# Kernel tuning notes

Hardware: AMD Instinct MI355X
Metric: run time of the kernel (lower is better)

The kernel has to match this reference:

```python
import jax, jax.numpy as jnp
import numpy as np


def setup_inputs() -> dict:
    key = jax.random.key(0)
    ks = jax.random.split(key, 5)
    b, l, ns, ni, d = 128, 64, 32, 16, 256
    scale = 1.0 / np.sqrt(d)
    return {
        "token_features": jax.random.normal(ks[0], (b, l, d), jnp.float32),
        "w_route_ws": jax.random.normal(ks[1], (l, ns, d), jnp.float32) * scale,
        "w_pose_ws": jax.random.normal(ks[2], (l, ns, d, d), jnp.float32) * scale,
        "w_route_si": jax.random.normal(ks[3], (ns, ni, d), jnp.float32) * scale,
        "w_pose_si": jax.random.normal(ks[4], (ns, ni, d, d), jnp.float32) * scale,
    }


def reference(token_features, w_route_ws, w_pose_ws, w_route_si, w_pose_si):
    d_model = token_features.shape[-1]

    # ---- route words -> slots ----
    # token activations ('norm' strategy): mean over d_model -> (b, l)
    a_words = jnp.sum(token_features, axis=-1) / d_model
    # routing logits (b, l, n_slot_caps), softmax over slot caps
    c_ws = jax.nn.softmax(jnp.einsum('lnj,blj->bln', w_route_ws, token_features), axis=-1)
    weighted_c = jnp.einsum('bls,bl->bs', c_ws, a_words)            # (b, ns)
    a_slots = weighted_c / jnp.sum(a_words, axis=-1, keepdims=True)  # (b, ns)
    # pose votes (b, l, ns, d) then weighted aggregation + divisive normalization
    u_hat_slots = jnp.einsum('lnij,blj->blni', w_pose_ws, token_features)
    u_slots = jnp.einsum('bls,bl,blsk->bsk', c_ws, a_words, u_hat_slots) / weighted_c[:, :, None]

    # ---- route slots -> intents ----
    c_si = jax.nn.softmax(jnp.einsum('sij,bsj->bsi', w_route_si, u_slots), axis=-1)
    weighted_c2 = jnp.einsum('bsi,bs->bi', c_si, a_slots)            # (b, ni)
    a_intents = weighted_c2 / jnp.sum(a_slots, axis=-1, keepdims=True)
    u_hat_intents = jnp.einsum('sijk,bsk->bsik', w_pose_si, u_slots)  # (b, ns, ni, d)
    u_intents = jnp.einsum('bsi,bs,bsik->bik', c_si, a_slots, u_hat_intents) / weighted_c2[:, :, None]

    return a_slots, u_slots, a_intents, u_intents
```

## Files before the change

kernel.cpp:

```cpp
#include <hip/hip_runtime.h>
#include <math.h>

#define B  128
#define L  64
#define NS 32
#define NI 16
#define D  256

typedef __attribute__((ext_vector_type(8))) short bf16x8;
typedef __attribute__((ext_vector_type(4))) float f32x4;

__device__ __forceinline__ float wave_reduce_sum(float v) {
#pragma unroll
  for (int off = 32; off; off >>= 1) v += __shfl_xor(v, off, 64);
  return v;
}
__device__ __forceinline__ float wave_reduce_max(float v) {
#pragma unroll
  for (int off = 32; off; off >>= 1) v = fmaxf(v, __shfl_xor(v, off, 64));
  return v;
}

__device__ __forceinline__ uint cvt_pk_bf16(float a, float b) {
  uint r;
  asm("v_cvt_pk_bf16_f32 %0, %1, %2" : "=v"(r) : "v"(a), "v"(b));
  return r;
}
__device__ __forceinline__ void split4(float4 v, uint2& h, uint2& lo) {
  h.x = cvt_pk_bf16(v.x, v.y);
  h.y = cvt_pk_bf16(v.z, v.w);
  float h0 = __uint_as_float(h.x << 16);
  float h1 = __uint_as_float(h.x & 0xFFFF0000u);
  float h2 = __uint_as_float(h.y << 16);
  float h3 = __uint_as_float(h.y & 0xFFFF0000u);
  lo.x = cvt_pk_bf16(v.x - h0, v.y - h1);
  lo.y = cvt_pk_bf16(v.z - h2, v.w - h3);
}

#define LGKM_BARRIER()                                   \
  do {                                                   \
    asm volatile("s_waitcnt lgkmcnt(0)" ::: "memory");   \
    __builtin_amdgcn_s_barrier();                        \
    asm volatile("" ::: "memory");                       \
  } while (0)

__device__ __forceinline__ int swzA(int row, int kcol) {
  int byte = (row << 7) + (kcol << 1);
  byte ^= (row & 7) << 4;
  return byte >> 1;
}

__global__ __launch_bounds__(256) void k1_route_words(
    const float* __restrict__ tf, const float* __restrict__ wr,
    float* __restrict__ wlsT, float* __restrict__ a_words) {
  int bl = blockIdx.x;
  int b  = bl >> 6;
  int l  = bl & (L - 1);
  int t  = threadIdx.x;
  int wave = t >> 6, lane = t & 63;
  __shared__ float sx[D];
  __shared__ float slog[NS];
  __shared__ float s_aw;
  sx[t] = tf[bl * D + t];
  __syncthreads();
  const float* wbase = wr + l * NS * D;
#pragma unroll
  for (int r = 0; r < 8; ++r) {
    int n = wave * 8 + r;
    const float* w = wbase + n * D;
    float p = 0.f;
#pragma unroll
    for (int jj = 0; jj < 4; ++jj) {
      int j = lane + jj * 64;
      p = fmaf(w[j], sx[j], p);
    }
    p = wave_reduce_sum(p);
    if (lane == 0) slog[n] = p;
  }
  if (wave == 0) {
    float p = sx[lane] + sx[lane + 64] + sx[lane + 128] + sx[lane + 192];
    p = wave_reduce_sum(p);
    if (lane == 0) s_aw = p * (1.f / D);
  }
  __syncthreads();
  if (wave == 0) {
    float aw = s_aw;
    float v = (lane < NS) ? slog[lane] : -INFINITY;
    float m = wave_reduce_max(v);
    float e = (lane < NS) ? __expf(v - m) : 0.f;
    float s = wave_reduce_sum(e);
    if (lane < NS) wlsT[(l * NS + lane) * B + b] = (e / s) * aw;
    if (lane == 0) a_words[bl] = aw;
  }
}

__global__ __launch_bounds__(64) void k2_slots_agg(
    const float* __restrict__ wlsT, const float* __restrict__ a_words,
    float* __restrict__ weighted_c, float* __restrict__ a_slots) {
  int b = blockIdx.x;
  int lane = threadIdx.x;
  float aw = a_words[b * L + lane];
  float sa = wave_reduce_sum(aw);
  if (lane < NS) {
    float wc = 0.f;
    for (int l = 0; l < L; ++l) wc += wlsT[(l * NS + lane) * B + b];
    weighted_c[b * NS + lane] = wc;
    a_slots[b * NS + lane] = wc / sa;
  }
}

__global__ __launch_bounds__(256, 4) void k3_mfma(
    const float* __restrict__ tf, const float* __restrict__ wp,
    const float* __restrict__ wlsT, float* __restrict__ part, int nsplit) {
  __shared__ ushort Ah[128 * 64], Al[128 * 64];

  int bx  = blockIdx.x;
  int t   = threadIdx.x;
  int sp  = bx % nsplit;
  int rem = bx / nsplit;
  int it  = rem & 3;
  int s   = rem >> 2;
  int i0  = it * 64;
  int lchunk = L / nsplit;
  int l0     = sp * lchunk;
  int steps  = lchunk * 4;

  int lane = t & 63, wn = t >> 6;
  int fr = lane & 15, q = lane >> 4;
  int rw = t >> 4, jq = (t & 15) * 4;

  f32x4 acc[8];
#pragma unroll
  for (int mi = 0; mi < 8; ++mi) acc[mi] = (f32x4)0.f;

  const size_t wlo = (size_t)(i0 + wn * 16 + fr) * D + q * 8;

  float4 rW[4];
  auto loadW = [&](int step) {
    if (step >= steps) step = steps - 1;
    int l  = l0 + (step >> 2);
    int jc = (step & 3) * 64;
    const float* wb = wp + ((size_t)l * NS + s) * (D * D) + wlo + jc;
    rW[0] = *(const float4*)(wb);
    rW[1] = *(const float4*)(wb + 4);
    rW[2] = *(const float4*)(wb + 32);
    rW[3] = *(const float4*)(wb + 36);
  };
  loadW(0);

  for (int step = 0; step < steps; ++step) {
    int l  = l0 + (step >> 2);
    int jc = (step & 3) * 64;
    const float* ab = tf + (size_t)l * D + jc + jq;
    const float* sb = wlsT + ((size_t)l * NS + s) * B;
#pragma unroll
    for (int p = 0; p < 8; ++p) {
      int bb = p * 16 + rw;
      float4 v = *(const float4*)(ab + (size_t)bb * (L * D));
      float sc = sb[bb];
      v.x *= sc; v.y *= sc; v.z *= sc; v.w *= sc;
      uint2 h, lo;
      split4(v, h, lo);
      *(uint2*)&Ah[swzA(bb, jq)] = h;
      *(uint2*)&Al[swzA(bb, jq)] = lo;
    }
    bf16x8 bh[2], bl[2];
#pragma unroll
    for (int k2 = 0; k2 < 2; ++k2) {
      uint2 h0, l0u, h1, l1u;
      split4(rW[k2 * 2], h0, l0u);
      split4(rW[k2 * 2 + 1], h1, l1u);
      uint4 hu = {h0.x, h0.y, h1.x, h1.y};
      uint4 lu = {l0u.x, l0u.y, l1u.x, l1u.y};
      bh[k2] = __builtin_bit_cast(bf16x8, hu);
      bl[k2] = __builtin_bit_cast(bf16x8, lu);
    }
    loadW(step + 1);
    LGKM_BARRIER();
#pragma unroll
    for (int k2 = 0; k2 < 2; ++k2) {
      int kb = k2 * 32 + q * 8;
#pragma unroll
      for (int mi = 0; mi < 8; ++mi) {
        bf16x8 ah = *(const bf16x8*)&Ah[swzA(mi * 16 + fr, kb)];
        bf16x8 al = *(const bf16x8*)&Al[swzA(mi * 16 + fr, kb)];
        acc[mi] = __builtin_amdgcn_mfma_f32_16x16x32_bf16(ah, bh[k2], acc[mi], 0, 0, 0);
        acc[mi] = __builtin_amdgcn_mfma_f32_16x16x32_bf16(ah, bl[k2], acc[mi], 0, 0, 0);
        acc[mi] = __builtin_amdgcn_mfma_f32_16x16x32_bf16(al, bh[k2], acc[mi], 0, 0, 0);
      }
    }
    LGKM_BARRIER();
  }

  float* pout = part + ((size_t)sp * NS + s) * (B * D);
  int col = i0 + wn * 16 + fr;
#pragma unroll
  for (int mi = 0; mi < 8; ++mi)
#pragma unroll
    for (int r = 0; r < 4; ++r) {
      int bb = mi * 16 + q * 4 + r;
      pout[(size_t)bb * D + col] = acc[mi][r];
    }
}

__global__ __launch_bounds__(256) void k3r_reduce(
    const float* __restrict__ part, const float* __restrict__ wc,
    float* __restrict__ u_slots, int nsplit) {
  int idx = blockIdx.x * 256 + threadIdx.x;
  int i  = idx & (D - 1);
  int sb = idx >> 8;
  int b  = sb & (B - 1);
  int s  = sb >> 7;
  float v = 0.f;
  for (int sp = 0; sp < nsplit; ++sp)
    v += part[(size_t)sp * (NS * B * D) + idx];
  u_slots[((size_t)b * NS + s) * D + i] = v / wc[b * NS + s];
}

__global__ __launch_bounds__(64) void k4_route_si(
    const float* __restrict__ u_slots, const float* __restrict__ wr_si,
    const float* __restrict__ a_slots, float* __restrict__ w2) {
  int bs = blockIdx.x;
  int s  = bs & (NS - 1);
  int lane = threadIdx.x;
  __shared__ float su[D];
  __shared__ float slog[NI];
#pragma unroll
  for (int jj = 0; jj < 4; ++jj) su[lane + jj * 64] = u_slots[bs * D + lane + jj * 64];
  __syncthreads();
  for (int i = 0; i < NI; ++i) {
    const float* w = wr_si + (s * NI + i) * D;
    float p = 0.f;
#pragma unroll
    for (int jj = 0; jj < 4; ++jj) {
      int j = lane + jj * 64;
      p = fmaf(w[j], su[j], p);
    }
    p = wave_reduce_sum(p);
    if (lane == 0) slog[i] = p;
  }
  __syncthreads();
  float v = (lane < NI) ? slog[lane] : -INFINITY;
  float m = wave_reduce_max(v);
  float e = (lane < NI) ? __expf(v - m) : 0.f;
  float ssum = wave_reduce_sum(e);
  if (lane < NI) w2[bs * NI + lane] = (e / ssum) * a_slots[bs];
}

__global__ __launch_bounds__(64) void k5_intents_agg(
    const float* __restrict__ w2, const float* __restrict__ a_slots,
    float* __restrict__ wc2, float* __restrict__ a_intents) {
  int b = blockIdx.x;
  int lane = threadIdx.x;
  float as = (lane < NS) ? a_slots[b * NS + lane] : 0.f;
  float sas = wave_reduce_sum(as);
  if (lane < NI) {
    float wc = 0.f;
    for (int s = 0; s < NS; ++s) wc += w2[(b * NS + s) * NI + lane];
    wc2[b * NI + lane] = wc;
    a_intents[b * NI + lane] = wc / sas;
  }
}

__global__ __launch_bounds__(256) void k6_wsum(
    const float* __restrict__ wps, float* __restrict__ wsum) {
  __shared__ float red[4][D];
  int si = blockIdx.x;
  int t  = threadIdx.x;
  int k4 = (t & 63) * 4;
  int jg = t >> 6;
  const float* base = wps + (size_t)si * D * D;
  float4 acc = {0.f, 0.f, 0.f, 0.f};
  for (int j = jg; j < D; j += 4) {
    float4 v = *(const float4*)(base + (size_t)j * D + k4);
    acc.x += v.x; acc.y += v.y; acc.z += v.z; acc.w += v.w;
  }
  *(float4*)&red[jg][k4] = acc;
  __syncthreads();
  wsum[si * D + t] = (red[0][t] + red[1][t]) + (red[2][t] + red[3][t]);
}

__global__ __launch_bounds__(256) void k7_uintents(
    const float* __restrict__ u_slots, const float* __restrict__ w2,
    const float* __restrict__ wsum, const float* __restrict__ wc2,
    float* __restrict__ u_intents) {
  int bi = blockIdx.x;
  int b = bi >> 4, i = bi & (NI - 1);
  int k = threadIdx.x;
  float acc = 0.f;
  for (int s = 0; s < NS; ++s) {
    float w = w2[(b * NS + s) * NI + i];
    acc = fmaf(w * u_slots[(b * NS + s) * D + k], wsum[(s * NI + i) * D + k], acc);
  }
  u_intents[bi * D + k] = acc / wc2[bi];
}

extern "C" void kernel_launch(void* const* d_in, const int* in_sizes, int n_in,
                              void* d_out, int out_size, void* d_ws, size_t ws_size,
                              hipStream_t stream) {
  const float* tf    = (const float*)d_in[0];
  const float* wr_ws = (const float*)d_in[1];
  const float* wp_ws = (const float*)d_in[2];
  const float* wr_si = (const float*)d_in[3];
  const float* wp_si = (const float*)d_in[4];

  float* out       = (float*)d_out;
  float* a_slots   = out;
  float* u_slots   = a_slots + B * NS;
  float* a_intents = u_slots + B * NS * D;
  float* u_intents = a_intents + B * NI;

  float* ws         = (float*)d_ws;
  float* wlsT       = ws;
  float* a_words    = wlsT + L * NS * B;
  float* weighted_c = a_words + B * L;
  float* w2         = weighted_c + B * NS;
  float* wc2        = w2 + B * NS * NI;
  float* wsum       = wc2 + B * NI;
  float* part       = wsum + NS * NI * D;

  const size_t base_f  = 473088;
  const size_t chunk_f = (size_t)NS * B * D;
  size_t avail_f = ws_size / sizeof(float);
  int nsplit = 1;
  if (avail_f >= base_f + 8 * chunk_f)      nsplit = 8;
  else if (avail_f >= base_f + 4 * chunk_f) nsplit = 4;
  else if (avail_f >= base_f + 2 * chunk_f) nsplit = 2;

  k1_route_words<<<B * L, 256, 0, stream>>>(tf, wr_ws, wlsT, a_words);
  k2_slots_agg<<<B, 64, 0, stream>>>(wlsT, a_words, weighted_c, a_slots);
  k3_mfma<<<128 * nsplit, 256, 0, stream>>>(tf, wp_ws, wlsT, part, nsplit);
  k3r_reduce<<<(NS * B * D) / 256, 256, 0, stream>>>(part, weighted_c, u_slots, nsplit);
  k6_wsum<<<NS * NI, 256, 0, stream>>>(wp_si, wsum);
  k4_route_si<<<B * NS, 64, 0, stream>>>(u_slots, wr_si, a_slots, w2);
  k5_intents_agg<<<B, 64, 0, stream>>>(w2, a_slots, wc2, a_intents);
  k7_uintents<<<B * NI, 256, 0, stream>>>(u_slots, w2, wsum, wc2, u_intents);
}
```

Before: 277.6 us.

## Merge wsum reduction into MFMA kernel and double-buffer A tiles with 2x2 warp tiling

The pose-vote MFMA kernel now also carries the independent w_pose_si column-sum blocks, interleaved in one grid, so that memory-bound reduction can overlap with the compute-bound GEMM and one launch disappears. The GEMM is restructured with double-buffered LDS A tiles and register-prefetched A and W for two steps ahead. A 2x2 wave tiling (64 rows x 32 cols per wave) replaces the 128x16 per-wave layout to improve reuse. The L split drops from 8 to 4 and occupancy from 4 to 2 blocks per CU, which trades parallelism and latency hiding for more register buffering.

```diff
diff --git a/kernel.cpp b/kernel.cpp
--- a/kernel.cpp
+++ b/kernel.cpp
@@ -109,15 +109,51 @@
   }
 }
 
-__global__ __launch_bounds__(256, 4) void k3_mfma(
+#define ATILE 8192
+
+__global__ __launch_bounds__(256, 2) void k3k6(
     const float* __restrict__ tf, const float* __restrict__ wp,
-    const float* __restrict__ wlsT, float* __restrict__ part, int nsplit) {
-  __shared__ ushort Ah[128 * 64], Al[128 * 64];
-
-  int bx  = blockIdx.x;
-  int t   = threadIdx.x;
-  int sp  = bx % nsplit;
-  int rem = bx / nsplit;
+    const float* __restrict__ wlsT, const float* __restrict__ wps,
+    float* __restrict__ part, float* __restrict__ wsum,
+    int nsplit, int nk3) {
+  union Smem {
+    struct { ushort Ah[2 * ATILE], Al[2 * ATILE]; } k3;
+    struct { float red[4][D]; } k6;
+  };
+  __shared__ Smem sm;
+
+  int bx = blockIdx.x;
+  int t  = threadIdx.x;
+
+  bool isK6;
+  int idx;
+  if (nk3 == 512) {
+    isK6 = (bx & 1);
+    idx  = bx >> 1;
+  } else {
+    isK6 = bx < NS * NI;
+    idx  = isK6 ? bx : bx - NS * NI;
+  }
+
+  if (isK6) {
+    int si = idx;
+    int k4 = (t & 63) * 4;
+    int jg = t >> 6;
+    const float* base = wps + (size_t)si * D * D;
+    float4 acc = {0.f, 0.f, 0.f, 0.f};
+    for (int j = jg; j < D; j += 4) {
+      float4 v = *(const float4*)(base + (size_t)j * D + k4);
+      acc.x += v.x; acc.y += v.y; acc.z += v.z; acc.w += v.w;
+    }
+    *(float4*)&sm.k6.red[jg][k4] = acc;
+    __syncthreads();
+    wsum[si * D + t] = (sm.k6.red[0][t] + sm.k6.red[1][t]) +
+                       (sm.k6.red[2][t] + sm.k6.red[3][t]);
+    return;
+  }
+
+  int sp  = idx % nsplit;
+  int rem = idx / nsplit;
   int it  = rem & 3;
   int s   = rem >> 2;
   int i0  = it * 64;
@@ -125,81 +161,122 @@
   int l0     = sp * lchunk;
   int steps  = lchunk * 4;
 
-  int lane = t & 63, wn = t >> 6;
+  int lane = t & 63, wv = t >> 6;
+  int wm = wv >> 1, wn = wv & 1;
   int fr = lane & 15, q = lane >> 4;
   int rw = t >> 4, jq = (t & 15) * 4;
 
-  f32x4 acc[8];
-#pragma unroll
-  for (int mi = 0; mi < 8; ++mi) acc[mi] = (f32x4)0.f;
-
-  const size_t wlo = (size_t)(i0 + wn * 16 + fr) * D + q * 8;
-
-  float4 rW[4];
-  auto loadW = [&](int step) {
+  f32x4 acc[4][2];
+#pragma unroll
+  for (int mi = 0; mi < 4; ++mi)
+#pragma unroll
+    for (int ni = 0; ni < 2; ++ni) acc[mi][ni] = (f32x4)0.f;
+
+  float4 rA[8];
+  float  rS[8];
+  float4 rWa[8], rWb[8];
+
+  auto loadA = [&](int step) {
     if (step >= steps) step = steps - 1;
-    int l  = l0 + (step >> 2);
-    int jc = (step & 3) * 64;
-    const float* wb = wp + ((size_t)l * NS + s) * (D * D) + wlo + jc;
-    rW[0] = *(const float4*)(wb);
-    rW[1] = *(const float4*)(wb + 4);
-    rW[2] = *(const float4*)(wb + 32);
-    rW[3] = *(const float4*)(wb + 36);
-  };
-  loadW(0);
-
-  for (int step = 0; step < steps; ++step) {
-    int l  = l0 + (step >> 2);
-    int jc = (step & 3) * 64;
+    int l = l0 + (step >> 2), jc = (step & 3) * 64;
     const float* ab = tf + (size_t)l * D + jc + jq;
     const float* sb = wlsT + ((size_t)l * NS + s) * B;
 #pragma unroll
     for (int p = 0; p < 8; ++p) {
       int bb = p * 16 + rw;
-      float4 v = *(const float4*)(ab + (size_t)bb * (L * D));
-      float sc = sb[bb];
+      rA[p] = *(const float4*)(ab + (size_t)bb * (L * D));
+      rS[p] = sb[bb];
+    }
+  };
+  auto loadW = [&](int step, float4 (&rW)[8]) {
+    if (step >= steps) step = steps - 1;
+    int l = l0 + (step >> 2), jc = (step & 3) * 64;
+    const float* w0 = wp + ((size_t)l * NS + s) * (D * D) + jc + q * 8;
+#pragma unroll
+    for (int ni = 0; ni < 2; ++ni) {
+      const float* wr_ = w0 + (size_t)(i0 + wn * 32 + ni * 16 + fr) * D;
+#pragma unroll
+      for (int k2 = 0; k2 < 2; ++k2) {
+        rW[k2 * 4 + ni * 2 + 0] = *(const float4*)(wr_ + k2 * 32);
+        rW[k2 * 4 + ni * 2 + 1] = *(const float4*)(wr_ + k2 * 32 + 4);
+      }
+    }
+  };
+  auto stageA = [&](int wofs) {
+#pragma unroll
+    for (int p = 0; p < 8; ++p) {
+      int bb = p * 16 + rw;
+      float4 v = rA[p];
+      float sc = rS[p];
       v.x *= sc; v.y *= sc; v.z *= sc; v.w *= sc;
       uint2 h, lo;
       split4(v, h, lo);
-      *(uint2*)&Ah[swzA(bb, jq)] = h;
-      *(uint2*)&Al[swzA(bb, jq)] = lo;
-    }
-    bf16x8 bh[2], bl[2];
+      int ix = swzA(bb, jq);
+      *(uint2*)&sm.k3.Ah[wofs + ix] = h;
+      *(uint2*)&sm.k3.Al[wofs + ix] = lo;
+    }
+  };
+  auto mfmaStep = [&](const float4 (&rW)[8], int rofs) {
 #pragma unroll
     for (int k2 = 0; k2 < 2; ++k2) {
-      uint2 h0, l0u, h1, l1u;
-      split4(rW[k2 * 2], h0, l0u);
-      split4(rW[k2 * 2 + 1], h1, l1u);
-      uint4 hu = {h0.x, h0.y, h1.x, h1.y};
-      uint4 lu = {l0u.x, l0u.y, l1u.x, l1u.y};
-      bh[k2] = __builtin_bit_cast(bf16x8, hu);
-      bl[k2] = __builtin_bit_cast(bf16x8, lu);
-    }
-    loadW(step + 1);
+      bf16x8 bh[2], bl[2];
+#pragma unroll
+      for (int ni = 0; ni < 2; ++ni) {
+        uint2 h0, e0, h1, e1;
+        split4(rW[k2 * 4 + ni * 2 + 0], h0, e0);
+        split4(rW[k2 * 4 + ni * 2 + 1], h1, e1);
+        uint4 hu = {h0.x, h0.y, h1.x, h1.y};
+        uint4 lu = {e0.x, e0.y, e1.x, e1.y};
+        bh[ni] = __builtin_bit_cast(bf16x8, hu);
+        bl[ni] = __builtin_bit_cast(bf16x8, lu);
+      }
+      int kb = k2 * 32 + q * 8;
+#pragma unroll
+      for (int mi = 0; mi < 4; ++mi) {
+        int ix = swzA(wm * 64 + mi * 16 + fr, kb);
+        bf16x8 ah = *(const bf16x8*)&sm.k3.Ah[rofs + ix];
+        bf16x8 al = *(const bf16x8*)&sm.k3.Al[rofs + ix];
+#pragma unroll
+        for (int ni = 0; ni < 2; ++ni) {
+          acc[mi][ni] = __builtin_amdgcn_mfma_f32_16x16x32_bf16(ah, bh[ni], acc[mi][ni], 0, 0, 0);
+          acc[mi][ni] = __builtin_amdgcn_mfma_f32_16x16x32_bf16(ah, bl[ni], acc[mi][ni], 0, 0, 0);
+          acc[mi][ni] = __builtin_amdgcn_mfma_f32_16x16x32_bf16(al, bh[ni], acc[mi][ni], 0, 0, 0);
+        }
+      }
+    }
+  };
+
+  loadA(0);
+  loadW(0, rWa);
+  loadW(1, rWb);
+  stageA(0);
+  loadA(1);
+  LGKM_BARRIER();
+
+  for (int tt = 0; tt < steps; tt += 2) {
+    mfmaStep(rWa, 0);
+    stageA(ATILE);
+    loadA(tt + 2);
+    loadW(tt + 2, rWa);
     LGKM_BARRIER();
-#pragma unroll
-    for (int k2 = 0; k2 < 2; ++k2) {
-      int kb = k2 * 32 + q * 8;
-#pragma unroll
-      for (int mi = 0; mi < 8; ++mi) {
-        bf16x8 ah = *(const bf16x8*)&Ah[swzA(mi * 16 + fr, kb)];
-        bf16x8 al = *(const bf16x8*)&Al[swzA(mi * 16 + fr, kb)];
-        acc[mi] = __builtin_amdgcn_mfma_f32_16x16x32_bf16(ah, bh[k2], acc[mi], 0, 0, 0);
-        acc[mi] = __builtin_amdgcn_mfma_f32_16x16x32_bf16(ah, bl[k2], acc[mi], 0, 0, 0);
-        acc[mi] = __builtin_amdgcn_mfma_f32_16x16x32_bf16(al, bh[k2], acc[mi], 0, 0, 0);
+    mfmaStep(rWb, ATILE);
+    stageA(0);
+    loadA(tt + 3);
+    loadW(tt + 3, rWb);
+    LGKM_BARRIER();
+  }
+
+  float* pout = part + ((size_t)sp * NS + s) * (B * D);
+#pragma unroll
+  for (int mi = 0; mi < 4; ++mi)
+#pragma unroll
+    for (int ni = 0; ni < 2; ++ni) {
+      int col = i0 + wn * 32 + ni * 16 + fr;
+#pragma unroll
+      for (int r = 0; r < 4; ++r) {
+        int bb = wm * 64 + mi * 16 + q * 4 + r;
+        pout[(size_t)bb * D + col] = acc[mi][ni][r];
       }
-    }
-    LGKM_BARRIER();
-  }
-
-  float* pout = part + ((size_t)sp * NS + s) * (B * D);
-  int col = i0 + wn * 16 + fr;
-#pragma unroll
-  for (int mi = 0; mi < 8; ++mi)
-#pragma unroll
-    for (int r = 0; r < 4; ++r) {
-      int bb = mi * 16 + q * 4 + r;
-      pout[(size_t)bb * D + col] = acc[mi][r];
     }
 }
 
@@ -262,24 +339,6 @@
   }
 }
 
-__global__ __launch_bounds__(256) void k6_wsum(
-    const float* __restrict__ wps, float* __restrict__ wsum) {
-  __shared__ float red[4][D];
-  int si = blockIdx.x;
-  int t  = threadIdx.x;
-  int k4 = (t & 63) * 4;
-  int jg = t >> 6;
-  const float* base = wps + (size_t)si * D * D;
-  float4 acc = {0.f, 0.f, 0.f, 0.f};
-  for (int j = jg; j < D; j += 4) {
-    float4 v = *(const float4*)(base + (size_t)j * D + k4);
-    acc.x += v.x; acc.y += v.y; acc.z += v.z; acc.w += v.w;
-  }
-  *(float4*)&red[jg][k4] = acc;
-  __syncthreads();
-  wsum[si * D + t] = (red[0][t] + red[1][t]) + (red[2][t] + red[3][t]);
-}
-
 __global__ __launch_bounds__(256) void k7_uintents(
     const float* __restrict__ u_slots, const float* __restrict__ w2,
     const float* __restrict__ wsum, const float* __restrict__ wc2,
@@ -323,15 +382,17 @@
   const size_t chunk_f = (size_t)NS * B * D;
   size_t avail_f = ws_size / sizeof(float);
   int nsplit = 1;
-  if (avail_f >= base_f + 8 * chunk_f)      nsplit = 8;
-  else if (avail_f >= base_f + 4 * chunk_f) nsplit = 4;
+  if (avail_f >= base_f + 4 * chunk_f)      nsplit = 4;
   else if (avail_f >= base_f + 2 * chunk_f) nsplit = 2;
+
+  int nk3  = 128 * nsplit;
+  int grid = nk3 + NS * NI;
 
   k1_route_words<<<B * L, 256, 0, stream>>>(tf, wr_ws, wlsT, a_words);
   k2_slots_agg<<<B, 64, 0, stream>>>(wlsT, a_words, weighted_c, a_slots);
-  k3_mfma<<<128 * nsplit, 256, 0, stream>>>(tf, wp_ws, wlsT, part, nsplit);
+  k3k6<<<grid, 256, 0, stream>>>(tf, wp_ws, wlsT, wp_si, part, wsum,
+                                 nsplit, nk3);
   k3r_reduce<<<(NS * B * D) / 256, 256, 0, stream>>>(part, weighted_c, u_slots, nsplit);
-  k6_wsum<<<NS * NI, 256, 0, stream>>>(wp_si, wsum);
   k4_route_si<<<B * NS, 64, 0, stream>>>(u_slots, wr_si, a_slots, w2);
   k5_intents_agg<<<B, 64, 0, stream>>>(w2, a_slots, wc2, a_intents);
   k7_uintents<<<B * NI, 256, 0, stream>>>(u_slots, w2, wsum, wc2, u_intents);
```

Measured after the change: 464.5 us. 1.67x slower.

## Pre-split token features to bf16 once and DMA tiles into LDS

Applied to the files above, without the earlier changes.

Adds a prepass kernel that splits token features into hi/lo bf16 tiles in pre-swizzled layout. The main MFMA kernel then copies these tiles into LDS with global_load_lds instead of converting per block. The per-(b,l) routing scale moves out of the A operand and is applied once per l on the accumulators. Each wave now computes a 64x32 output tile (2x2 wave grid) instead of 128x16, giving more operand reuse. The max split count drops from 8 to 4, which cuts parallelism but also halves partial-sum traffic. It adds an extra kernel launch and workspace, and the old register prefetch of W across steps is gone.

```diff
diff --git a/kernel.cpp b/kernel.cpp
--- a/kernel.cpp
+++ b/kernel.cpp
@@ -37,17 +37,39 @@
   lo.y = cvt_pk_bf16(v.z - h2, v.w - h3);
 }
 
-#define LGKM_BARRIER()                                   \
-  do {                                                   \
-    asm volatile("s_waitcnt lgkmcnt(0)" ::: "memory");   \
-    __builtin_amdgcn_s_barrier();                        \
-    asm volatile("" ::: "memory");                       \
-  } while (0)
+__device__ __forceinline__ void dma16(const void* g, void* l) {
+  __builtin_amdgcn_global_load_lds(
+      (const __attribute__((address_space(1))) void*)g,
+      (__attribute__((address_space(3))) void*)l, 16, 0, 0);
+}
 
 __device__ __forceinline__ int swzA(int row, int kcol) {
   int byte = (row << 7) + (kcol << 1);
   byte ^= (row & 7) << 4;
   return byte >> 1;
+}
+
+__global__ __launch_bounds__(256) void kx_split(
+    const float* __restrict__ tf, ushort* __restrict__ xh,
+    ushort* __restrict__ xl) {
+  int tile = blockIdx.x;
+  int l  = tile >> 2;
+  int jc = (tile & 3) * 64;
+  int t  = threadIdx.x;
+  int row = t >> 1;
+  int k0  = (t & 1) * 32;
+  const float* src = tf + ((size_t)row * L + l) * D + jc + k0;
+  ushort* ht = xh + (size_t)tile * 8192;
+  ushort* lt = xl + (size_t)tile * 8192;
+#pragma unroll
+  for (int c = 0; c < 8; ++c) {
+    float4 v = *(const float4*)(src + c * 4);
+    uint2 h, lo;
+    split4(v, h, lo);
+    int ix = swzA(row, k0 + c * 4);
+    *(uint2*)&ht[ix] = h;
+    *(uint2*)&lt[ix] = lo;
+  }
 }
 
 __global__ __launch_bounds__(256) void k1_route_words(
@@ -109,13 +131,14 @@
   }
 }
 
-__global__ __launch_bounds__(256, 4) void k3_mfma(
-    const float* __restrict__ tf, const float* __restrict__ wp,
-    const float* __restrict__ wlsT, float* __restrict__ part, int nsplit) {
-  __shared__ ushort Ah[128 * 64], Al[128 * 64];
+__global__ __launch_bounds__(256) void k3_mfma(
+    const ushort* __restrict__ xh, const ushort* __restrict__ xl,
+    const float* __restrict__ wp, const float* __restrict__ wlsT,
+    float* __restrict__ part, int nsplit) {
+  __shared__ ushort Ah[8192], Al[8192];
+  __shared__ float sw[128];
 
   int bx  = blockIdx.x;
-  int t   = threadIdx.x;
   int sp  = bx % nsplit;
   int rem = bx / nsplit;
   int it  = rem & 3;
@@ -125,81 +148,98 @@
   int l0     = sp * lchunk;
   int steps  = lchunk * 4;
 
-  int lane = t & 63, wn = t >> 6;
+  int t = threadIdx.x;
+  int lane = t & 63, wv = t >> 6;
+  int wm = wv >> 1, wn = wv & 1;
   int fr = lane & 15, q = lane >> 4;
-  int rw = t >> 4, jq = (t & 15) * 4;
-
-  f32x4 acc[8];
-#pragma unroll
-  for (int mi = 0; mi < 8; ++mi) acc[mi] = (f32x4)0.f;
-
-  const size_t wlo = (size_t)(i0 + wn * 16 + fr) * D + q * 8;
-
-  float4 rW[4];
-  auto loadW = [&](int step) {
-    if (step >= steps) step = steps - 1;
-    int l  = l0 + (step >> 2);
-    int jc = (step & 3) * 64;
-    const float* wb = wp + ((size_t)l * NS + s) * (D * D) + wlo + jc;
-    rW[0] = *(const float4*)(wb);
-    rW[1] = *(const float4*)(wb + 4);
-    rW[2] = *(const float4*)(wb + 32);
-    rW[3] = *(const float4*)(wb + 36);
-  };
-  loadW(0);
+
+  f32x4 P[4][2], R[4][2];
+#pragma unroll
+  for (int mi = 0; mi < 4; ++mi)
+#pragma unroll
+    for (int ni = 0; ni < 2; ++ni) { P[mi][ni] = (f32x4)0.f; R[mi][ni] = (f32x4)0.f; }
 
   for (int step = 0; step < steps; ++step) {
-    int l  = l0 + (step >> 2);
-    int jc = (step & 3) * 64;
-    const float* ab = tf + (size_t)l * D + jc + jq;
-    const float* sb = wlsT + ((size_t)l * NS + s) * B;
-#pragma unroll
-    for (int p = 0; p < 8; ++p) {
-      int bb = p * 16 + rw;
-      float4 v = *(const float4*)(ab + (size_t)bb * (L * D));
-      float sc = sb[bb];
-      v.x *= sc; v.y *= sc; v.z *= sc; v.w *= sc;
-      uint2 h, lo;
-      split4(v, h, lo);
-      *(uint2*)&Ah[swzA(bb, jq)] = h;
-      *(uint2*)&Al[swzA(bb, jq)] = lo;
-    }
-    bf16x8 bh[2], bl[2];
-#pragma unroll
-    for (int k2 = 0; k2 < 2; ++k2) {
-      uint2 h0, l0u, h1, l1u;
-      split4(rW[k2 * 2], h0, l0u);
-      split4(rW[k2 * 2 + 1], h1, l1u);
-      uint4 hu = {h0.x, h0.y, h1.x, h1.y};
-      uint4 lu = {l0u.x, l0u.y, l1u.x, l1u.y};
-      bh[k2] = __builtin_bit_cast(bf16x8, hu);
-      bl[k2] = __builtin_bit_cast(bf16x8, lu);
-    }
-    loadW(step + 1);
-    LGKM_BARRIER();
+    int l   = l0 + (step >> 2);
+    int jci = step & 3;
+    size_t tile = ((size_t)l * 4 + jci) * 8192;
+    const ushort* th = xh + tile;
+    const ushort* tl = xl + tile;
+#pragma unroll
+    for (int ii = 0; ii < 4; ++ii) {
+      int ofs = (wv * 4 + ii) * 512;
+      dma16(th + ofs + lane * 8, &Ah[ofs]);
+      dma16(tl + ofs + lane * 8, &Al[ofs]);
+    }
+    int jc = jci * 64;
+    float4 rW[8];
+    const float* wb = wp + ((size_t)l * NS + s) * (D * D) + jc + q * 8;
+#pragma unroll
+    for (int ni = 0; ni < 2; ++ni) {
+      const float* wr_ = wb + (size_t)(i0 + wn * 32 + ni * 16 + fr) * D;
+#pragma unroll
+      for (int k2 = 0; k2 < 2; ++k2) {
+        rW[(ni * 2 + k2) * 2 + 0] = *(const float4*)(wr_ + k2 * 32);
+        rW[(ni * 2 + k2) * 2 + 1] = *(const float4*)(wr_ + k2 * 32 + 4);
+      }
+    }
+    if (jci == 0 && t < 128) sw[t] = wlsT[((size_t)l * NS + s) * B + t];
+    __syncthreads();
+
+    bf16x8 bh[2][2], bl[2][2];
+#pragma unroll
+    for (int ni = 0; ni < 2; ++ni)
+#pragma unroll
+      for (int k2 = 0; k2 < 2; ++k2) {
+        uint2 h0, e0, h1, e1;
+        split4(rW[(ni * 2 + k2) * 2 + 0], h0, e0);
+        split4(rW[(ni * 2 + k2) * 2 + 1], h1, e1);
+        uint4 hu = {h0.x, h0.y, h1.x, h1.y};
+        uint4 lu = {e0.x, e0.y, e1.x, e1.y};
+        bh[ni][k2] = __builtin_bit_cast(bf16x8, hu);
+        bl[ni][k2] = __builtin_bit_cast(bf16x8, lu);
+      }
 #pragma unroll
     for (int k2 = 0; k2 < 2; ++k2) {
       int kb = k2 * 32 + q * 8;
 #pragma unroll
-      for (int mi = 0; mi < 8; ++mi) {
-        bf16x8 ah = *(const bf16x8*)&Ah[swzA(mi * 16 + fr, kb)];
-        bf16x8 al = *(const bf16x8*)&Al[swzA(mi * 16 + fr, kb)];
-        acc[mi] = __builtin_amdgcn_mfma_f32_16x16x32_bf16(ah, bh[k2], acc[mi], 0, 0, 0);
-        acc[mi] = __builtin_amdgcn_mfma_f32_16x16x32_bf16(ah, bl[k2], acc[mi], 0, 0, 0);
-        acc[mi] = __builtin_amdgcn_mfma_f32_16x16x32_bf16(al, bh[k2], acc[mi], 0, 0, 0);
-      }
-    }
-    LGKM_BARRIER();
+      for (int mi = 0; mi < 4; ++mi) {
+        int ix = swzA(wm * 64 + mi * 16 + fr, kb);
+        bf16x8 ah = *(const bf16x8*)&Ah[ix];
+        bf16x8 al = *(const bf16x8*)&Al[ix];
+#pragma unroll
+        for (int ni = 0; ni < 2; ++ni) {
+          P[mi][ni] = __builtin_amdgcn_mfma_f32_16x16x32_bf16(ah, bh[ni][k2], P[mi][ni], 0, 0, 0);
+          P[mi][ni] = __builtin_amdgcn_mfma_f32_16x16x32_bf16(ah, bl[ni][k2], P[mi][ni], 0, 0, 0);
+          P[mi][ni] = __builtin_amdgcn_mfma_f32_16x16x32_bf16(al, bh[ni][k2], P[mi][ni], 0, 0, 0);
+        }
+      }
+    }
+    if (jci == 3) {
+#pragma unroll
+      for (int mi = 0; mi < 4; ++mi) {
+        f32x4 s4 = *(const f32x4*)&sw[wm * 64 + mi * 16 + q * 4];
+#pragma unroll
+        for (int ni = 0; ni < 2; ++ni) {
+          R[mi][ni] += s4 * P[mi][ni];
+          P[mi][ni] = (f32x4)0.f;
+        }
+      }
+    }
+    __syncthreads();
   }
 
   float* pout = part + ((size_t)sp * NS + s) * (B * D);
-  int col = i0 + wn * 16 + fr;
-#pragma unroll
-  for (int mi = 0; mi < 8; ++mi)
-#pragma unroll
-    for (int r = 0; r < 4; ++r) {
-      int bb = mi * 16 + q * 4 + r;
-      pout[(size_t)bb * D + col] = acc[mi][r];
+#pragma unroll
+  for (int mi = 0; mi < 4; ++mi)
+#pragma unroll
+    for (int ni = 0; ni < 2; ++ni) {
+      int col = i0 + wn * 32 + ni * 16 + fr;
+#pragma unroll
+      for (int r = 0; r < 4; ++r) {
+        int bb = wm * 64 + mi * 16 + q * 4 + r;
+        pout[(size_t)bb * D + col] = R[mi][ni][r];
+      }
     }
 }
 
@@ -317,19 +357,21 @@
   float* w2         = weighted_c + B * NS;
   float* wc2        = w2 + B * NS * NI;
   float* wsum       = wc2 + B * NI;
-  float* part       = wsum + NS * NI * D;
-
-  const size_t base_f  = 473088;
+  ushort* xh        = (ushort*)(wsum + NS * NI * D);
+  ushort* xl        = xh + (size_t)L * 4 * 8192;
+  float*  part      = (float*)(xl + (size_t)L * 4 * 8192);
+
+  const size_t base_f  = 473088 + 1048576 * 2 / 2 * 2;
   const size_t chunk_f = (size_t)NS * B * D;
   size_t avail_f = ws_size / sizeof(float);
   int nsplit = 1;
-  if (avail_f >= base_f + 8 * chunk_f)      nsplit = 8;
-  else if (avail_f >= base_f + 4 * chunk_f) nsplit = 4;
+  if (avail_f >= base_f + 4 * chunk_f)      nsplit = 4;
   else if (avail_f >= base_f + 2 * chunk_f) nsplit = 2;
 
+  kx_split<<<L * 4, 256, 0, stream>>>(tf, xh, xl);
   k1_route_words<<<B * L, 256, 0, stream>>>(tf, wr_ws, wlsT, a_words);
   k2_slots_agg<<<B, 64, 0, stream>>>(wlsT, a_words, weighted_c, a_slots);
-  k3_mfma<<<128 * nsplit, 256, 0, stream>>>(tf, wp_ws, wlsT, part, nsplit);
+  k3_mfma<<<NS * 4 * nsplit, 256, 0, stream>>>(xh, xl, wp_ws, wlsT, part, nsplit);
   k3r_reduce<<<(NS * B * D) / 256, 256, 0, stream>>>(part, weighted_c, u_slots, nsplit);
   k6_wsum<<<NS * NI, 256, 0, stream>>>(wp_si, wsum);
   k4_route_si<<<B * NS, 64, 0, stream>>>(u_slots, wr_si, a_slots, w2);
```

Result: slower. 297.0 us (median of 2 runs) (+7.0%).
